# Kernel tuning notes

Hardware: AMD Instinct MI355X
Metric: run time of the kernel (lower is better)

## Reference

```python
import jax, jax.numpy as jnp
import numpy as np


def sinusoidal_pe(d, length, dtype=jnp.float32):
    """Standard transformer sin/cos positional encoding along the W axis.
    Returns (d, length): pe[2i, p] = sin(p/10000^(2i/d)), pe[2i+1, p] = cos(...)."""
    pos = jnp.arange(length, dtype=dtype)[None, :]            # (1, W)
    i = jnp.arange(0, d, 2, dtype=dtype)[:, None]             # (d//2, 1)
    div = jnp.exp(-i * (np.log(10000.0) / d))                 # (d//2, 1)
    ang = pos * div                                           # (d//2, W)
    pe = jnp.zeros((d, length), dtype)
    pe = pe.at[0::2].set(jnp.sin(ang)).at[1::2].set(jnp.cos(ang))
    return pe


def setup_inputs() -> dict:
    key = jax.random.key(0)
    ks = jax.random.split(key, 8)
    B, C, D, H, W = 2, 64, 32, 64, 96
    q_k_dim = 32
    s = 1.0 / np.sqrt(C)
    return {
        "x": jax.random.normal(ks[0], (B, C, D, H, W), jnp.float32),
        "Wq": jax.random.normal(ks[1], (q_k_dim, C), jnp.float32) * s,
        "bq": jax.random.normal(ks[2], (q_k_dim,), jnp.float32) * 0.01,
        "Wk": jax.random.normal(ks[3], (q_k_dim, C), jnp.float32) * s,
        "bk": jax.random.normal(ks[4], (q_k_dim,), jnp.float32) * 0.01,
        "Wv": jax.random.normal(ks[5], (C, C), jnp.float32) * s,
        "bv": jax.random.normal(ks[6], (C,), jnp.float32) * 0.01,
        "gamma": jax.random.normal(ks[7], (1,), jnp.float32) * 0.1,
    }


def reference(x, Wq, bq, Wk, bk, Wv, bv, gamma):
    # x: (B, C, D, H, W)
    B, C, D, H, W = x.shape
    qk = Wq.shape[0]
    # 1x1x1 Conv3d == per-voxel channel matmul
    Q = jnp.einsum('bcdhw,qc->bqdhw', x, Wq) + bq[None, :, None, None, None]
    K = jnp.einsum('bcdhw,qc->bqdhw', x, Wk) + bk[None, :, None, None, None]
    V = jnp.einsum('bcdhw,vc->bvdhw', x, Wv) + bv[None, :, None, None, None]
    # additive sinusoidal positional encoding along the row (W) axis
    pe_qk = sinusoidal_pe(qk, W, x.dtype)[None, :, None, None, :]
    pe_v = sinusoidal_pe(C, W, x.dtype)[None, :, None, None, :]
    Q = Q + pe_qk
    K = K + pe_qk
    V = V + pe_v
    # row attention: scores over the W axis, independently per (b, d, h)
    # attn[b,d,h,i,j] = sum_q Q[b,q,d,h,i] * K[b,q,d,h,j]  (no 1/sqrt(d) scaling, as in source)
    attn = jax.nn.softmax(jnp.einsum('bqdhi,bqdhj->bdhij', Q, K), axis=-1)
    # out[b,c,d,h,i] = sum_j V[b,c,d,h,j] * attn[b,d,h,i,j]
    out = jnp.einsum('bcdhj,bdhij->bcdhi', V, attn)
    return gamma * out + x
```

## Files before the change

### kernel.cpp

```cpp
#include <hip/hip_runtime.h>
#include <hip/hip_bf16.h>
#include <math.h>

constexpr int Cc = 64, Dd = 32, Hh = 64, Ww = 96, QKd = 32;
constexpr int CSTRIDE = Dd * Hh * Ww;
constexpr int BDIM = 256;

#define FREQ_QK 0.28782313662425574f
#define FREQ_V  0.14391156831212787f

typedef __bf16 bf16_t;
typedef bf16_t bf16x8 __attribute__((ext_vector_type(8)));
typedef bf16_t bf16x4 __attribute__((ext_vector_type(4)));
typedef float  floatx4 __attribute__((ext_vector_type(4)));

constexpr int XS_STRIDE = 72;
constexpr int QS_STRIDE = 40;
constexpr int VS_STRIDE = 104;
constexpr int PS_STRIDE = 104;
constexpr int OFF_QS = 9984;
constexpr int OFF_KS = 9984 + 3840;
constexpr int OFF_VS = 9984 + 7680;
constexpr int SMEM_ELEMS = 9984 + 7680 + 6656;

__global__ __launch_bounds__(BDIM, 3)
void row_attn_mfma(const float* __restrict__ x,
                   const float* __restrict__ Wq, const float* __restrict__ bq,
                   const float* __restrict__ Wk, const float* __restrict__ bk,
                   const float* __restrict__ Wv, const float* __restrict__ bv,
                   const float* __restrict__ gamma,
                   float* __restrict__ y)
{
    __shared__ __align__(16) bf16_t smem[SMEM_ELEMS];
    bf16_t* Xs = smem;
    bf16_t* Ps = smem;
    bf16_t* Qs = smem + OFF_QS;
    bf16_t* Ks = smem + OFF_KS;
    bf16_t* Vs = smem + OFF_VS;

    const int t    = threadIdx.x;
    const int lane = t & 63;
    const int wid  = t >> 6;
    const int l16  = lane & 15;
    const int quad = lane >> 4;

    const int bid = blockIdx.x;
    const int b   = bid / (Dd * Hh);
    const int rem = bid % (Dd * Hh);
    const int d   = rem / Hh;
    const int h   = rem % Hh;
    const int base0 = b * (Cc * CSTRIDE) + d * (Hh * Ww) + h * Ww;

#pragma unroll
    for (int k = 0; k < 12; ++k) {
        int idx = t + k * BDIM;
        int w  = idx % Ww;
        int c  = (idx / Ww) * 2;
        float v0 = x[base0 + c * CSTRIDE + w];
        float v1 = x[base0 + (c + 1) * CSTRIDE + w];
        unsigned short u0 = __builtin_bit_cast(unsigned short, (bf16_t)v0);
        unsigned short u1 = __builtin_bit_cast(unsigned short, (bf16_t)v1);
        *(unsigned int*)(&Xs[w * XS_STRIDE + c]) = (unsigned)u0 | ((unsigned)u1 << 16);
    }

    const float* Wmat = (wid == 0) ? Wq : (wid == 1) ? Wk : Wv;
    const float* bias = (wid == 0) ? bq : (wid == 1) ? bk : bv;
    const float freqc = (wid < 2) ? FREQ_QK : FREQ_V;
    const int   mbase = (wid == 3) ? 32 : 0;

    bf16x8 wfrag[2][2];
#pragma unroll
    for (int mt = 0; mt < 2; ++mt)
#pragma unroll
        for (int kt = 0; kt < 2; ++kt) {
            const float* p = Wmat + (mbase + mt * 16 + l16) * 64 + kt * 32 + quad * 8;
            float4 lo = *(const float4*)p;
            float4 hi = *(const float4*)(p + 4);
            bf16x8 f;
            f[0] = (bf16_t)lo.x; f[1] = (bf16_t)lo.y; f[2] = (bf16_t)lo.z; f[3] = (bf16_t)lo.w;
            f[4] = (bf16_t)hi.x; f[5] = (bf16_t)hi.y; f[6] = (bf16_t)hi.z; f[7] = (bf16_t)hi.w;
            wfrag[mt][kt] = f;
        }
    float biasv[2][4], freq2[2][2];
#pragma unroll
    for (int mt = 0; mt < 2; ++mt) {
#pragma unroll
        for (int r = 0; r < 4; ++r)
            biasv[mt][r] = bias[mbase + mt * 16 + quad * 4 + r];
#pragma unroll
        for (int p2 = 0; p2 < 2; ++p2)
            freq2[mt][p2] = __expf(-(float)(mbase + mt * 16 + quad * 4 + 2 * p2) * freqc);
    }
    __syncthreads();

    bf16_t* dstQK = (wid == 0) ? Qs : Ks;
#pragma unroll
    for (int nt = 0; nt < 6; ++nt) {
        bf16x8 bfr[2];
#pragma unroll
        for (int kt = 0; kt < 2; ++kt)
            bfr[kt] = *(const bf16x8*)(&Xs[(nt * 16 + l16) * XS_STRIDE + kt * 32 + quad * 8]);
#pragma unroll
        for (int mt = 0; mt < 2; ++mt) {
            floatx4 acc = {0.f, 0.f, 0.f, 0.f};
            acc = __builtin_amdgcn_mfma_f32_16x16x32_bf16(wfrag[mt][0], bfr[0], acc, 0, 0, 0);
            acc = __builtin_amdgcn_mfma_f32_16x16x32_bf16(wfrag[mt][1], bfr[1], acc, 0, 0, 0);
            float wv = (float)(nt * 16 + l16);
            float out[4];
#pragma unroll
            for (int p2 = 0; p2 < 2; ++p2) {
                float sn, cs;
                __sincosf(wv * freq2[mt][p2], &sn, &cs);
                out[2 * p2]     = acc[2 * p2]     + biasv[mt][2 * p2]     + sn;
                out[2 * p2 + 1] = acc[2 * p2 + 1] + biasv[mt][2 * p2 + 1] + cs;
            }
            if (wid < 2) {
                bf16x4 pk;
                pk[0] = (bf16_t)out[0]; pk[1] = (bf16_t)out[1];
                pk[2] = (bf16_t)out[2]; pk[3] = (bf16_t)out[3];
                *(bf16x4*)(&dstQK[(nt * 16 + l16) * QS_STRIDE + mt * 16 + quad * 4]) = pk;
            } else {
#pragma unroll
                for (int r = 0; r < 4; ++r)
                    Vs[(mbase + mt * 16 + quad * 4 + r) * VS_STRIDE + nt * 16 + l16] = (bf16_t)out[r];
            }
        }
    }
    __syncthreads();

    const int it0 = (wid < 2) ? wid * 2 : wid + 2;
    const int itc = (wid < 2) ? 2 : 1;
    for (int ii = 0; ii < itc; ++ii) {
        const int it = it0 + ii;
        bf16x8 afr = *(const bf16x8*)(&Qs[(it * 16 + l16) * QS_STRIDE + quad * 8]);
        floatx4 sacc[6];
#pragma unroll
        for (int jt = 0; jt < 6; ++jt) {
            bf16x8 bfr = *(const bf16x8*)(&Ks[(jt * 16 + l16) * QS_STRIDE + quad * 8]);
            floatx4 z = {0.f, 0.f, 0.f, 0.f};
            sacc[jt] = __builtin_amdgcn_mfma_f32_16x16x32_bf16(afr, bfr, z, 0, 0, 0);
        }
#pragma unroll
        for (int r = 0; r < 4; ++r) {
            float m = sacc[0][r];
#pragma unroll
            for (int jt = 1; jt < 6; ++jt) m = fmaxf(m, sacc[jt][r]);
#pragma unroll
            for (int msk = 1; msk < 16; msk <<= 1) m = fmaxf(m, __shfl_xor(m, msk));
            float e[6], sum = 0.f;
#pragma unroll
            for (int jt = 0; jt < 6; ++jt) { e[jt] = __expf(sacc[jt][r] - m); sum += e[jt]; }
#pragma unroll
            for (int msk = 1; msk < 16; msk <<= 1) sum += __shfl_xor(sum, msk);
            float inv = 1.0f / sum;
            int row = it * 16 + quad * 4 + r;
#pragma unroll
            for (int jt = 0; jt < 6; ++jt)
                Ps[row * PS_STRIDE + jt * 16 + l16] = (bf16_t)(e[jt] * inv);
        }
    }
    __syncthreads();

    const float g = gamma[0];
    const int ct = wid;
    bf16x8 vfr[3];
#pragma unroll
    for (int ks = 0; ks < 3; ++ks)
        vfr[ks] = *(const bf16x8*)(&Vs[(ct * 16 + l16) * VS_STRIDE + ks * 32 + quad * 8]);
#pragma unroll
    for (int it = 0; it < 6; ++it) {
        floatx4 acc = {0.f, 0.f, 0.f, 0.f};
#pragma unroll
        for (int ks = 0; ks < 3; ++ks) {
            bf16x8 bfr = *(const bf16x8*)(&Ps[(it * 16 + l16) * PS_STRIDE + ks * 32 + quad * 8]);
            acc = __builtin_amdgcn_mfma_f32_16x16x32_bf16(vfr[ks], bfr, acc, 0, 0, 0);
        }
#pragma unroll
        for (int r = 0; r < 4; ++r) {
            int c  = ct * 16 + quad * 4 + r;
            int gi = base0 + c * CSTRIDE + it * 16 + l16;
            y[gi] = fmaf(g, acc[r], x[gi]);
        }
    }
}

extern "C" void kernel_launch(void* const* d_in, const int* in_sizes, int n_in,
                              void* d_out, int out_size, void* d_ws, size_t ws_size,
                              hipStream_t stream) {
    const float* x     = (const float*)d_in[0];
    const float* Wq    = (const float*)d_in[1];
    const float* bq    = (const float*)d_in[2];
    const float* Wk    = (const float*)d_in[3];
    const float* bk    = (const float*)d_in[4];
    const float* Wv    = (const float*)d_in[5];
    const float* bv    = (const float*)d_in[6];
    const float* gamma = (const float*)d_in[7];
    float* y = (float*)d_out;

    dim3 grid(2 * 32 * 64);
    row_attn_mfma<<<grid, BDIM, 0, stream>>>(x, Wq, bq, Wk, bk, Wv, bv, gamma, y);
}
```

Measured before the change: 215.6 us.

## Load x fragments directly, fuse softmax with PV per wave, drop shared X tile

```diff
diff --git a/kernel.cpp b/kernel.cpp
--- a/kernel.cpp
+++ b/kernel.cpp
@@ -14,27 +14,34 @@
 typedef bf16_t bf16x4 __attribute__((ext_vector_type(4)));
 typedef float  floatx4 __attribute__((ext_vector_type(4)));
 
-constexpr int XS_STRIDE = 72;
 constexpr int QS_STRIDE = 40;
-constexpr int VS_STRIDE = 104;
-constexpr int PS_STRIDE = 104;
-constexpr int OFF_QS = 9984;
-constexpr int OFF_KS = 9984 + 3840;
-constexpr int OFF_VS = 9984 + 7680;
-constexpr int SMEM_ELEMS = 9984 + 7680 + 6656;
-
-__global__ __launch_bounds__(BDIM, 3)
-void row_attn_mfma(const float* __restrict__ x,
-                   const float* __restrict__ Wq, const float* __restrict__ bq,
-                   const float* __restrict__ Wk, const float* __restrict__ bk,
-                   const float* __restrict__ Wv, const float* __restrict__ bv,
-                   const float* __restrict__ gamma,
-                   float* __restrict__ y)
+constexpr int VS_STRIDE = 100;
+constexpr int PS_STRIDE = 100;
+constexpr int OFF_KS = 96 * QS_STRIDE;
+constexpr int OFF_VS = 2 * 96 * QS_STRIDE;
+constexpr int OFF_PS = OFF_VS + 64 * VS_STRIDE;
+constexpr int PS_WAVE = 16 * PS_STRIDE;
+constexpr int SMEM_ELEMS = OFF_PS + 4 * PS_WAVE;
+
+__device__ inline bf16x8 ld_frag64(const bf16_t* p) {
+    bf16x4 lo = *(const bf16x4*)p;
+    bf16x4 hi = *(const bf16x4*)(p + 4);
+    bf16x8 f;
+    f[0] = lo[0]; f[1] = lo[1]; f[2] = lo[2]; f[3] = lo[3];
+    f[4] = hi[0]; f[5] = hi[1]; f[6] = hi[2]; f[7] = hi[3];
+    return f;
+}
+
+__global__ __launch_bounds__(BDIM, 4)
+void row_attn_v3(const float* __restrict__ x,
+                 const float* __restrict__ Wq, const float* __restrict__ bq,
+                 const float* __restrict__ Wk, const float* __restrict__ bk,
+                 const float* __restrict__ Wv, const float* __restrict__ bv,
+                 const float* __restrict__ gamma,
+                 float* __restrict__ y)
 {
     __shared__ __align__(16) bf16_t smem[SMEM_ELEMS];
-    bf16_t* Xs = smem;
-    bf16_t* Ps = smem;
-    bf16_t* Qs = smem + OFF_QS;
+    bf16_t* Qs = smem;
     bf16_t* Ks = smem + OFF_KS;
     bf16_t* Vs = smem + OFF_VS;
 
@@ -43,6 +50,7 @@
     const int wid  = t >> 6;
     const int l16  = lane & 15;
     const int quad = lane >> 4;
+    bf16_t* Psw = smem + OFF_PS + wid * PS_WAVE;
 
     const int bid = blockIdx.x;
     const int b   = bid / (Dd * Hh);
@@ -50,18 +58,7 @@
     const int d   = rem / Hh;
     const int h   = rem % Hh;
     const int base0 = b * (Cc * CSTRIDE) + d * (Hh * Ww) + h * Ww;
-
-#pragma unroll
-    for (int k = 0; k < 12; ++k) {
-        int idx = t + k * BDIM;
-        int w  = idx % Ww;
-        int c  = (idx / Ww) * 2;
-        float v0 = x[base0 + c * CSTRIDE + w];
-        float v1 = x[base0 + (c + 1) * CSTRIDE + w];
-        unsigned short u0 = __builtin_bit_cast(unsigned short, (bf16_t)v0);
-        unsigned short u1 = __builtin_bit_cast(unsigned short, (bf16_t)v1);
-        *(unsigned int*)(&Xs[w * XS_STRIDE + c]) = (unsigned)u0 | ((unsigned)u1 << 16);
-    }
+    const float* xblk = x + base0;
 
     const float* Wmat = (wid == 0) ? Wq : (wid == 1) ? Wk : Wv;
     const float* bias = (wid == 0) ? bq : (wid == 1) ? bk : bv;
@@ -91,15 +88,19 @@
         for (int p2 = 0; p2 < 2; ++p2)
             freq2[mt][p2] = __expf(-(float)(mbase + mt * 16 + quad * 4 + 2 * p2) * freqc);
     }
-    __syncthreads();
 
     bf16_t* dstQK = (wid == 0) ? Qs : Ks;
 #pragma unroll
     for (int nt = 0; nt < 6; ++nt) {
         bf16x8 bfr[2];
 #pragma unroll
-        for (int kt = 0; kt < 2; ++kt)
-            bfr[kt] = *(const bf16x8*)(&Xs[(nt * 16 + l16) * XS_STRIDE + kt * 32 + quad * 8]);
+        for (int kt = 0; kt < 2; ++kt) {
+#pragma unroll
+            for (int j = 0; j < 8; ++j) {
+                int c = kt * 32 + quad * 8 + j;
+                bfr[kt][j] = (bf16_t)xblk[c * CSTRIDE + nt * 16 + l16];
+            }
+        }
 #pragma unroll
         for (int mt = 0; mt < 2; ++mt) {
             floatx4 acc = {0.f, 0.f, 0.f, 0.f};
@@ -128,10 +129,13 @@
     }
     __syncthreads();
 
+    const float g = gamma[0];
     const int it0 = (wid < 2) ? wid * 2 : wid + 2;
     const int itc = (wid < 2) ? 2 : 1;
+
     for (int ii = 0; ii < itc; ++ii) {
         const int it = it0 + ii;
+
         bf16x8 afr = *(const bf16x8*)(&Qs[(it * 16 + l16) * QS_STRIDE + quad * 8]);
         floatx4 sacc[6];
 #pragma unroll
@@ -153,33 +157,29 @@
 #pragma unroll
             for (int msk = 1; msk < 16; msk <<= 1) sum += __shfl_xor(sum, msk);
             float inv = 1.0f / sum;
-            int row = it * 16 + quad * 4 + r;
 #pragma unroll
             for (int jt = 0; jt < 6; ++jt)
-                Ps[row * PS_STRIDE + jt * 16 + l16] = (bf16_t)(e[jt] * inv);
-        }
-    }
-    __syncthreads();
-
-    const float g = gamma[0];
-    const int ct = wid;
-    bf16x8 vfr[3];
-#pragma unroll
-    for (int ks = 0; ks < 3; ++ks)
-        vfr[ks] = *(const bf16x8*)(&Vs[(ct * 16 + l16) * VS_STRIDE + ks * 32 + quad * 8]);
-#pragma unroll
-    for (int it = 0; it < 6; ++it) {
-        floatx4 acc = {0.f, 0.f, 0.f, 0.f};
-#pragma unroll
-        for (int ks = 0; ks < 3; ++ks) {
-            bf16x8 bfr = *(const bf16x8*)(&Ps[(it * 16 + l16) * PS_STRIDE + ks * 32 + quad * 8]);
-            acc = __builtin_amdgcn_mfma_f32_16x16x32_bf16(vfr[ks], bfr, acc, 0, 0, 0);
-        }
-#pragma unroll
-        for (int r = 0; r < 4; ++r) {
-            int c  = ct * 16 + quad * 4 + r;
-            int gi = base0 + c * CSTRIDE + it * 16 + l16;
-            y[gi] = fmaf(g, acc[r], x[gi]);
+                Psw[(quad * 4 + r) * PS_STRIDE + jt * 16 + l16] = (bf16_t)(e[jt] * inv);
+        }
+
+        bf16x8 pfr[3];
+#pragma unroll
+        for (int ks = 0; ks < 3; ++ks)
+            pfr[ks] = ld_frag64(&Psw[l16 * PS_STRIDE + ks * 32 + quad * 8]);
+#pragma unroll
+        for (int ct = 0; ct < 4; ++ct) {
+            floatx4 oacc = {0.f, 0.f, 0.f, 0.f};
+#pragma unroll
+            for (int ks = 0; ks < 3; ++ks) {
+                bf16x8 vfr = ld_frag64(&Vs[(ct * 16 + l16) * VS_STRIDE + ks * 32 + quad * 8]);
+                oacc = __builtin_amdgcn_mfma_f32_16x16x32_bf16(vfr, pfr[ks], oacc, 0, 0, 0);
+            }
+#pragma unroll
+            for (int r = 0; r < 4; ++r) {
+                int c  = ct * 16 + quad * 4 + r;
+                int gi = base0 + c * CSTRIDE + it * 16 + l16;
+                y[gi] = fmaf(g, oacc[r], x[gi]);
+            }
         }
     }
 }
@@ -198,5 +198,5 @@
     float* y = (float*)d_out;
 
     dim3 grid(2 * 32 * 64);
-    row_attn_mfma<<<grid, BDIM, 0, stream>>>(x, Wq, bq, Wk, bk, Wv, bv, gamma, y);
+    row_attn_v3<<<grid, BDIM, 0, stream>>>(x, Wq, bq, Wk, bk, Wv, bv, gamma, y);
 }
```

Measured after the change: 247.6 us. 14.8% more time.
